# Performance work log

Measured on AMD Instinct MI355X. Metric: run time of the kernel, lower is better.

The kernel has to match this reference:

```python
import jax, jax.numpy as jnp
import numpy as np

WIN_SIZE = 11
SIGMA = 1.5
DATA_RANGE = 255.0
C1 = (0.01 * DATA_RANGE) ** 2
C2 = (0.03 * DATA_RANGE) ** 2


def _gauss_1d():
    coords = np.arange(WIN_SIZE, dtype=np.float64) - WIN_SIZE // 2
    g = np.exp(-(coords ** 2) / (2.0 * SIGMA ** 2))
    g = g / g.sum()
    return jnp.asarray(g, dtype=jnp.float32)


def _blur(img, g):
    # Depthwise separable gaussian blur, VALID padding (pytorch_msssim style).
    C = img.shape[1]
    dn = ('NCHW', 'OIHW', 'NCHW')
    kh = jnp.tile(g.reshape(1, 1, WIN_SIZE, 1), (C, 1, 1, 1))  # [C,1,K,1]
    kw = jnp.tile(g.reshape(1, 1, 1, WIN_SIZE), (C, 1, 1, 1))  # [C,1,1,K]
    out = jax.lax.conv_general_dilated(img, kh, (1, 1), 'VALID',
                                       dimension_numbers=dn, feature_group_count=C)
    out = jax.lax.conv_general_dilated(out, kw, (1, 1), 'VALID',
                                       dimension_numbers=dn, feature_group_count=C)
    return out


def _ssim_mean(x, y):
    g = _gauss_1d()
    mu1 = _blur(x, g)
    mu2 = _blur(y, g)
    mu1_sq = mu1 * mu1
    mu2_sq = mu2 * mu2
    mu1_mu2 = mu1 * mu2
    sigma1_sq = _blur(x * x, g) - mu1_sq
    sigma2_sq = _blur(y * y, g) - mu2_sq
    sigma12 = _blur(x * y, g) - mu1_mu2
    cs_map = (2.0 * sigma12 + C2) / (sigma1_sq + sigma2_sq + C2)
    ssim_map = ((2.0 * mu1_mu2 + C1) / (mu1_sq + mu2_sq + C1)) * cs_map
    return jnp.mean(ssim_map)


def setup_inputs() -> dict:
    key = jax.random.key(0)
    kx, ky = jax.random.split(key)
    shape = (16, 3, 512, 512)
    x = jax.random.uniform(kx, shape, dtype=jnp.float32)
    y = jax.random.uniform(ky, shape, dtype=jnp.float32)
    return {"x": x, "y": y, "epoch": 1}


def reference(x, y, epoch):
    # forward computes a Charbonnier L1 too, but it is dead code:
    # loss = ssim_loss = 1 - SSIM(x, y)
    return 1.0 - _ssim_mean(x, y)
```

## Files before the change

### kernel.cpp

```cpp
#include <hip/hip_runtime.h>
#include <math.h>


#define HH 512
#define WW 512
#define NCH 48
#define OUTD 502
#define SEGS 16
#define SEG_ROWS 32
#define ITERS 44
#define NBLK (NCH * SEGS)

#define TWO_C1 13.0050f
#define TWO_C2 117.0450f

struct GW { float g[11]; };

__global__ __launch_bounds__(256, 2)
void ssim_main(const float* __restrict__ x, const float* __restrict__ y,
               float* __restrict__ partial, GW gw) {
    const int tid = threadIdx.x;
    const int bid = blockIdx.x;
    const int ch  = bid >> 4;
    const int seg = bid & (SEGS - 1);
    const int r0  = seg * SEG_ROWS;
    const int nrows = min(SEG_ROWS, OUTD - r0);

    int j = 2 * tid;
    const bool jvalid = (j < OUTD);
    if (!jvalid) j = 500;

    const size_t chbase = (size_t)ch * (HH * WW);
    const float* xb = x + chbase + j;
    const float* yb = y + chbase + j;

    float rP[11][2], rQ[11][2], rS[11][2], rT[11][2];
    float acc = 0.0f;

    for (int base = 0; base < ITERS; base += 11) {
        #pragma unroll
        for (int u = 0; u < 11; ++u) {
            const int it = base + u;
            const int r  = min(r0 + it, HH - 1);
            const float2* xr = (const float2*)(xb + (size_t)r * WW);
            const float2* yr = (const float2*)(yb + (size_t)r * WW);

            float p[12], q[12];
            #pragma unroll
            for (int d = 0; d < 6; ++d) {
                float2 xv = xr[d];
                float2 yv = yr[d];
                p[2*d]   = xv.x + yv.x;  q[2*d]   = xv.x - yv.x;
                p[2*d+1] = xv.y + yv.y;  q[2*d+1] = xv.y - yv.y;
            }
            float s[12], t[12];
            #pragma unroll
            for (int d = 0; d < 12; ++d) { s[d] = p[d]*p[d]; t[d] = q[d]*q[d]; }

            float hp0=0.f,hq0=0.f,hs0=0.f,ht0=0.f;
            float hp1=0.f,hq1=0.f,hs1=0.f,ht1=0.f;
            #pragma unroll
            for (int k = 0; k < 11; ++k) {
                const float w = gw.g[k];
                hp0 = fmaf(w, p[k],   hp0);  hq0 = fmaf(w, q[k],   hq0);
                hs0 = fmaf(w, s[k],   hs0);  ht0 = fmaf(w, t[k],   ht0);
                hp1 = fmaf(w, p[k+1], hp1);  hq1 = fmaf(w, q[k+1], hq1);
                hs1 = fmaf(w, s[k+1], hs1);  ht1 = fmaf(w, t[k+1], ht1);
            }
            rP[u][0]=hp0; rP[u][1]=hp1;  rQ[u][0]=hq0; rQ[u][1]=hq1;
            rS[u][0]=hs0; rS[u][1]=hs1;  rT[u][0]=ht0; rT[u][1]=ht1;

            const int il = it - 10;
            if (il >= 0 && il < nrows && jvalid) {
                float P0=0.f,Q0=0.f,S0=0.f,T0=0.f;
                float P1=0.f,Q1=0.f,S1=0.f,T1=0.f;
                #pragma unroll
                for (int k = 0; k < 11; ++k) {
                    const int sl = (u + 1 + k) % 11;
                    const float w = gw.g[k];
                    P0=fmaf(w,rP[sl][0],P0); Q0=fmaf(w,rQ[sl][0],Q0);
                    S0=fmaf(w,rS[sl][0],S0); T0=fmaf(w,rT[sl][0],T0);
                    P1=fmaf(w,rP[sl][1],P1); Q1=fmaf(w,rQ[sl][1],Q1);
                    S1=fmaf(w,rS[sl][1],S1); T1=fmaf(w,rT[sl][1],T1);
                }
                {
                    float A = P0*P0, B = Q0*Q0;
                    float u1 = A - B, u2 = A + B;
                    float ln_ = u1 + TWO_C1;
                    float ld_ = u2 + TWO_C1;
                    float cn_ = (S0 - T0) - u1 + TWO_C2;
                    float cd_ = (S0 + T0) - u2 + TWO_C2;
                    acc += (ln_ * cn_) / (ld_ * cd_);
                }
                {
                    float A = P1*P1, B = Q1*Q1;
                    float u1 = A - B, u2 = A + B;
                    float ln_ = u1 + TWO_C1;
                    float ld_ = u2 + TWO_C1;
                    float cn_ = (S1 - T1) - u1 + TWO_C2;
                    float cd_ = (S1 + T1) - u2 + TWO_C2;
                    acc += (ln_ * cn_) / (ld_ * cd_);
                }
            }
        }
    }

    #pragma unroll
    for (int off = 32; off > 0; off >>= 1) acc += __shfl_down(acc, off);
    __shared__ float sh[4];
    const int wid  = tid >> 6;
    const int lane = tid & 63;
    if (lane == 0) sh[wid] = acc;
    __syncthreads();
    if (tid == 0) partial[bid] = sh[0] + sh[1] + sh[2] + sh[3];
}

__global__ void ssim_reduce(const float* __restrict__ partial,
                            float* __restrict__ out) {
    double s = 0.0;
    for (int i = threadIdx.x; i < NBLK; i += 256) s += (double)partial[i];
    #pragma unroll
    for (int off = 32; off > 0; off >>= 1) s += __shfl_down(s, off);
    __shared__ double sh[4];
    const int wid  = threadIdx.x >> 6;
    const int lane = threadIdx.x & 63;
    if (lane == 0) sh[wid] = s;
    __syncthreads();
    if (threadIdx.x == 0) {
        double tot = sh[0] + sh[1] + sh[2] + sh[3];
        double cnt = (double)NCH * (double)OUTD * (double)OUTD;
        out[0] = (float)(1.0 - tot / cnt);
    }
}

extern "C" void kernel_launch(void* const* d_in, const int* in_sizes, int n_in,
                              void* d_out, int out_size, void* d_ws, size_t ws_size,
                              hipStream_t stream) {
    const float* x = (const float*)d_in[0];
    const float* y = (const float*)d_in[1];
    float* out = (float*)d_out;
    float* ws  = (float*)d_ws;

    GW gw;
    {
        double v[11], sum = 0.0;
        for (int k = 0; k < 11; ++k) {
            double c = (double)(k - 5);
            v[k] = exp(-(c * c) / 4.5);
            sum += v[k];
        }
        for (int k = 0; k < 11; ++k) gw.g[k] = (float)(v[k] / sum);
    }

    hipLaunchKernelGGL(ssim_main, dim3(NBLK), dim3(256), 0, stream, x, y, ws, gw);
    hipLaunchKernelGGL(ssim_reduce, dim3(1), dim3(256), 0, stream, ws, out);
}
```

Before: 197.7 us.

## Stage rows in double-buffered LDS and reshape segments to cut halo overhead

Each row of x and y is now loaded once per block with one coalesced float2 per thread. The sum and difference are written to a double-buffered LDS tile, and the horizontal 11-tap window is read from there instead of each thread issuing overlapping global loads. The row segments shrink to 23 rows across 22 segments per channel, so the 10-row halo is a larger share of each block but there are more blocks. The epilogue merges the two divisions into one fast __fdividef. The change adds a __syncthreads per row and uses approximate division, which can lower precision slightly.

New measurement: 169.3 us. -14.4%, faster.

```diff
diff --git a/kernel.cpp b/kernel.cpp
--- a/kernel.cpp
+++ b/kernel.cpp
@@ -6,102 +6,155 @@
 #define WW 512
 #define NCH 48
 #define OUTD 502
-#define SEGS 16
-#define SEG_ROWS 32
-#define ITERS 44
+#define SEGS 22
+#define SEG_ROWS 23
+#define ITERS 33
 #define NBLK (NCH * SEGS)
 
 #define TWO_C1 13.0050f
 #define TWO_C2 117.0450f
 
 struct GW { float g[11]; };
+
+#define HCHAIN(UU)                                                         \
+    {                                                                      \
+        float hp0=0.f,hq0=0.f,hs0=0.f,ht0=0.f;                             \
+        float hp1=0.f,hq1=0.f,hs1=0.f,ht1=0.f;                             \
+        _Pragma("unroll")                                                  \
+        for (int k = 0; k < 11; ++k) {                                     \
+            const float w = gw.g[k];                                       \
+            const float pk = p[k],   qk = q[k];                            \
+            const float pk1 = p[k+1], qk1 = q[k+1];                        \
+            hp0 = fmaf(w, pk,      hp0);  hq0 = fmaf(w, qk,      hq0);     \
+            hs0 = fmaf(w, pk*pk,   hs0);  ht0 = fmaf(w, qk*qk,   ht0);     \
+            hp1 = fmaf(w, pk1,     hp1);  hq1 = fmaf(w, qk1,     hq1);     \
+            hs1 = fmaf(w, pk1*pk1, hs1);  ht1 = fmaf(w, qk1*qk1, ht1);     \
+        }                                                                  \
+        rP[UU][0]=hp0; rP[UU][1]=hp1;  rQ[UU][0]=hq0; rQ[UU][1]=hq1;       \
+        rS[UU][0]=hs0; rS[UU][1]=hs1;  rT[UU][0]=ht0; rT[UU][1]=ht1;       \
+    }
+
+#define READ_WINDOW(PARX)                                                  \
+    float p[12], q[12];                                                    \
+    {                                                                      \
+        const float2* pb = (const float2*)&lds[PARX][0][0];                \
+        const float2* qb = (const float2*)&lds[PARX][1][0];                \
+        _Pragma("unroll")                                                  \
+        for (int k2 = 0; k2 < 6; ++k2) {                                   \
+            float2 pv = pb[tcol + k2];                                     \
+            float2 qv = qb[tcol + k2];                                     \
+            p[2*k2] = pv.x; p[2*k2+1] = pv.y;                              \
+            q[2*k2] = qv.x; q[2*k2+1] = qv.y;                              \
+        }                                                                  \
+    }
+
+#define STAGE_WRITE(PARX)                                                  \
+    {                                                                      \
+        float2 pw, qw;                                                     \
+        pw.x = nxv.x + nyv.x;  pw.y = nxv.y + nyv.y;                       \
+        qw.x = nxv.x - nyv.x;  qw.y = nxv.y - nyv.y;                       \
+        ((float2*)&lds[PARX][0][0])[tid] = pw;                             \
+        ((float2*)&lds[PARX][1][0])[tid] = qw;                             \
+    }
+
+#define VEPI(UU)                                                           \
+    {                                                                      \
+        float P0=0.f,Q0=0.f,Sv0=0.f,Tv0=0.f;                               \
+        float P1=0.f,Q1=0.f,Sv1=0.f,Tv1=0.f;                               \
+        _Pragma("unroll")                                                  \
+        for (int k = 0; k < 11; ++k) {                                     \
+            const int sl = ((UU) + 1 + k) % 11;                            \
+            const float w = gw.g[k];                                       \
+            P0=fmaf(w,rP[sl][0],P0);   Q0=fmaf(w,rQ[sl][0],Q0);            \
+            Sv0=fmaf(w,rS[sl][0],Sv0); Tv0=fmaf(w,rT[sl][0],Tv0);          \
+            P1=fmaf(w,rP[sl][1],P1);   Q1=fmaf(w,rQ[sl][1],Q1);            \
+            Sv1=fmaf(w,rS[sl][1],Sv1); Tv1=fmaf(w,rT[sl][1],Tv1);          \
+        }                                                                  \
+        float A0=P0*P0, B0=Q0*Q0;                                          \
+        float u10=A0-B0, u20=A0+B0;                                        \
+        float ln0=u10+TWO_C1, ld0=u20+TWO_C1;                              \
+        float cn0=(Sv0-Tv0)-u10+TWO_C2, cd0=(Sv0+Tv0)-u20+TWO_C2;          \
+        float A1=P1*P1, B1=Q1*Q1;                                          \
+        float u11=A1-B1, u21=A1+B1;                                        \
+        float ln1=u11+TWO_C1, ld1=u21+TWO_C1;                              \
+        float cn1=(Sv1-Tv1)-u11+TWO_C2, cd1=(Sv1+Tv1)-u21+TWO_C2;          \
+        float n0=ln0*cn0, d0=ld0*cd0;                                      \
+        float n1=ln1*cn1, d1=ld1*cd1;                                      \
+        float num=fmaf(n0,d1,n1*d0), den=d0*d1;                            \
+        float val=__fdividef(num,den);                                     \
+        if (jvalid) acc += val;                                            \
+    }
 
 __global__ __launch_bounds__(256, 2)
 void ssim_main(const float* __restrict__ x, const float* __restrict__ y,
                float* __restrict__ partial, GW gw) {
+    __shared__ float lds[2][2][WW];
+
     const int tid = threadIdx.x;
     const int bid = blockIdx.x;
-    const int ch  = bid >> 4;
-    const int seg = bid & (SEGS - 1);
+    const int ch  = bid / SEGS;
+    const int seg = bid - ch * SEGS;
     const int r0  = seg * SEG_ROWS;
     const int nrows = min(SEG_ROWS, OUTD - r0);
 
-    int j = 2 * tid;
-    const bool jvalid = (j < OUTD);
-    if (!jvalid) j = 500;
+    const bool jvalid = (tid < 251);
+    const int tcol = jvalid ? tid : 250;
 
     const size_t chbase = (size_t)ch * (HH * WW);
-    const float* xb = x + chbase + j;
-    const float* yb = y + chbase + j;
+    const float* xc = x + chbase;
+    const float* yc = y + chbase;
 
     float rP[11][2], rQ[11][2], rS[11][2], rT[11][2];
     float acc = 0.0f;
 
-    for (int base = 0; base < ITERS; base += 11) {
+    {
+        float2 nxv = ((const float2*)(xc + (size_t)r0 * WW))[tid];
+        float2 nyv = ((const float2*)(yc + (size_t)r0 * WW))[tid];
+        STAGE_WRITE(0)
+    }
+    __syncthreads();
+
+    #pragma unroll
+    for (int u = 0; u < 11; ++u) {
+        const int par = u & 1;
+        float2 nxv, nyv;
+        {
+            const int rn = r0 + u + 1;
+            nxv = ((const float2*)(xc + (size_t)rn * WW))[tid];
+            nyv = ((const float2*)(yc + (size_t)rn * WW))[tid];
+        }
+        READ_WINDOW(par)
+        HCHAIN(u)
+        if (u == 10) {
+            VEPI(10)
+        }
+        STAGE_WRITE(par ^ 1)
+        __syncthreads();
+    }
+
+    #pragma unroll 1
+    for (int blk = 1; blk < 3; ++blk) {
         #pragma unroll
         for (int u = 0; u < 11; ++u) {
-            const int it = base + u;
-            const int r  = min(r0 + it, HH - 1);
-            const float2* xr = (const float2*)(xb + (size_t)r * WW);
-            const float2* yr = (const float2*)(yb + (size_t)r * WW);
-
-            float p[12], q[12];
-            #pragma unroll
-            for (int d = 0; d < 6; ++d) {
-                float2 xv = xr[d];
-                float2 yv = yr[d];
-                p[2*d]   = xv.x + yv.x;  q[2*d]   = xv.x - yv.x;
-                p[2*d+1] = xv.y + yv.y;  q[2*d+1] = xv.y - yv.y;
+            const int it  = 11 * blk + u;
+            const int par = (blk + u) & 1;
+            const bool more = (it < ITERS - 1);
+            float2 nxv, nyv;
+            if (more) {
+                const int rn = min(r0 + it + 1, HH - 1);
+                nxv = ((const float2*)(xc + (size_t)rn * WW))[tid];
+                nyv = ((const float2*)(yc + (size_t)rn * WW))[tid];
             }
-            float s[12], t[12];
-            #pragma unroll
-            for (int d = 0; d < 12; ++d) { s[d] = p[d]*p[d]; t[d] = q[d]*q[d]; }
-
-            float hp0=0.f,hq0=0.f,hs0=0.f,ht0=0.f;
-            float hp1=0.f,hq1=0.f,hs1=0.f,ht1=0.f;
-            #pragma unroll
-            for (int k = 0; k < 11; ++k) {
-                const float w = gw.g[k];
-                hp0 = fmaf(w, p[k],   hp0);  hq0 = fmaf(w, q[k],   hq0);
-                hs0 = fmaf(w, s[k],   hs0);  ht0 = fmaf(w, t[k],   ht0);
-                hp1 = fmaf(w, p[k+1], hp1);  hq1 = fmaf(w, q[k+1], hq1);
-                hs1 = fmaf(w, s[k+1], hs1);  ht1 = fmaf(w, t[k+1], ht1);
+            READ_WINDOW(par)
+            HCHAIN(u)
+            const int il = it - 10;
+            if (il < nrows) {
+                VEPI(u)
             }
-            rP[u][0]=hp0; rP[u][1]=hp1;  rQ[u][0]=hq0; rQ[u][1]=hq1;
-            rS[u][0]=hs0; rS[u][1]=hs1;  rT[u][0]=ht0; rT[u][1]=ht1;
-
-            const int il = it - 10;
-            if (il >= 0 && il < nrows && jvalid) {
-                float P0=0.f,Q0=0.f,S0=0.f,T0=0.f;
-                float P1=0.f,Q1=0.f,S1=0.f,T1=0.f;
-                #pragma unroll
-                for (int k = 0; k < 11; ++k) {
-                    const int sl = (u + 1 + k) % 11;
-                    const float w = gw.g[k];
-                    P0=fmaf(w,rP[sl][0],P0); Q0=fmaf(w,rQ[sl][0],Q0);
-                    S0=fmaf(w,rS[sl][0],S0); T0=fmaf(w,rT[sl][0],T0);
-                    P1=fmaf(w,rP[sl][1],P1); Q1=fmaf(w,rQ[sl][1],Q1);
-                    S1=fmaf(w,rS[sl][1],S1); T1=fmaf(w,rT[sl][1],T1);
-                }
-                {
-                    float A = P0*P0, B = Q0*Q0;
-                    float u1 = A - B, u2 = A + B;
-                    float ln_ = u1 + TWO_C1;
-                    float ld_ = u2 + TWO_C1;
-                    float cn_ = (S0 - T0) - u1 + TWO_C2;
-                    float cd_ = (S0 + T0) - u2 + TWO_C2;
-                    acc += (ln_ * cn_) / (ld_ * cd_);
-                }
-                {
-                    float A = P1*P1, B = Q1*Q1;
-                    float u1 = A - B, u2 = A + B;
-                    float ln_ = u1 + TWO_C1;
-                    float ld_ = u2 + TWO_C1;
-                    float cn_ = (S1 - T1) - u1 + TWO_C2;
-                    float cd_ = (S1 + T1) - u2 + TWO_C2;
-                    acc += (ln_ * cn_) / (ld_ * cd_);
-                }
+            if (more) {
+                STAGE_WRITE(par ^ 1)
             }
+            __syncthreads();
         }
     }
 
```
